# Kernel tuning notes

Hardware: AMD Instinct MI355X
Metric: run time of the kernel (lower is better)

Reference implementation:

```python
import jax, jax.numpy as jnp
import numpy as np

N = 100000      # nodes
E = 1_000_000   # edges (avg degree ~10)
D_IN = 64
HID = 64
N_CLS = 32


def setup_inputs() -> dict:
    key = jax.random.key(0)
    ks = jax.random.split(key, 9)
    x = jax.random.normal(ks[0], (N, D_IN), dtype=jnp.float32)
    edge_index = jax.random.randint(ks[1], (2, E), 0, N, dtype=jnp.int32)
    s_in = 1.0 / np.sqrt(D_IN)
    s_h = 1.0 / np.sqrt(HID)
    W1 = jax.random.normal(ks[2], (D_IN, HID), dtype=jnp.float32) * s_in
    b1 = jnp.zeros((HID,), dtype=jnp.float32)
    W2 = jax.random.normal(ks[3], (HID, HID), dtype=jnp.float32) * s_h
    b2 = jnp.zeros((HID,), dtype=jnp.float32)
    Wl = jax.random.normal(ks[4], (HID, N_CLS), dtype=jnp.float32) * s_h
    bl = jnp.zeros((N_CLS,), dtype=jnp.float32)
    return {"x": x, "edge_index": edge_index,
            "W1": W1, "b1": b1, "W2": W2, "b2": b2, "Wl": Wl, "bl": bl}


def reference(x, edge_index, W1, b1, W2, b2, Wl, bl):
    # GCNConv default: add self-loops, symmetric normalization D^-1/2 (A+I) D^-1/2
    loop = jnp.arange(N, dtype=edge_index.dtype)
    src = jnp.concatenate([edge_index[0], loop])  # [E+N]
    dst = jnp.concatenate([edge_index[1], loop])  # [E+N]

    deg = jax.ops.segment_sum(jnp.ones_like(dst, dtype=jnp.float32), dst,
                              num_segments=N)              # [N]
    dinv = jnp.where(deg > 0, jax.lax.rsqrt(deg), 0.0)      # D^-1/2
    norm = dinv[src] * dinv[dst]                            # [E+N]

    def gcn_conv(h, W, b):
        h = h @ W                                           # [N, F_out]
        msg = h[src] * norm[:, None]                        # gather + scale
        return jax.ops.segment_sum(msg, dst, num_segments=N) + b

    h = jax.nn.relu(gcn_conv(x, W1, b1))
    h = jax.nn.relu(gcn_conv(h, W2, b2))
    return h @ Wl + bl
```

## Files before the change

kernel.cpp:

```cpp
#include <hip/hip_runtime.h>
#include <hip/hip_fp16.h>
#include <math.h>


#define TPB    256
#define TPB1   1024
#define EBLKS  256
#define BSH    7
#define BNODES (1 << BSH)
#define CAPSH  11
#define CAP    (1 << CAPSH)

__global__ __launch_bounds__(TPB1)
void k_scatter(const int* __restrict__ src, const int* __restrict__ dst,
               int* __restrict__ gcnt, int* __restrict__ ebuf,
               int E, int CH, int NBC) {
    __shared__ int h[1024];
    int tid = threadIdx.x, b = blockIdx.x;
    h[tid] = 0;
    __syncthreads();
    int beg = b * CH, end = min(E, beg + CH);
    if (beg < end) {
        int nfull = (end - beg) & ~3;
        for (int i = beg + tid * 4; i < beg + nfull; i += TPB1 * 4) {
            int4 d = *(const int4*)&dst[i];
            atomicAdd(&h[d.x >> BSH], 1);
            atomicAdd(&h[d.y >> BSH], 1);
            atomicAdd(&h[d.z >> BSH], 1);
            atomicAdd(&h[d.w >> BSH], 1);
        }
        if (tid < (end - beg) - nfull)
            atomicAdd(&h[dst[beg + nfull + tid] >> BSH], 1);
    }
    __syncthreads();
    for (int c = tid; c < NBC; c += TPB1) {
        int n = h[c];
        int base = (n > 0) ? atomicAdd(&gcnt[c], n) : 0;
        h[c] = (c << CAPSH) + base;
    }
    __syncthreads();
    if (beg >= end) return;
    int nfull = (end - beg) & ~3;
    for (int i = beg + tid * 4; i < beg + nfull; i += TPB1 * 4) {
        int4 s4 = *(const int4*)&src[i];
        int4 d4 = *(const int4*)&dst[i];
        int p0 = atomicAdd(&h[d4.x >> BSH], 1);
        int p1 = atomicAdd(&h[d4.y >> BSH], 1);
        int p2 = atomicAdd(&h[d4.z >> BSH], 1);
        int p3 = atomicAdd(&h[d4.w >> BSH], 1);
        ebuf[p0] = (s4.x << BSH) | (d4.x & (BNODES - 1));
        ebuf[p1] = (s4.y << BSH) | (d4.y & (BNODES - 1));
        ebuf[p2] = (s4.z << BSH) | (d4.z & (BNODES - 1));
        ebuf[p3] = (s4.w << BSH) | (d4.w & (BNODES - 1));
    }
    if (tid < (end - beg) - nfull) {
        int i = beg + nfull + tid;
        int d = dst[i];
        int p = atomicAdd(&h[d >> BSH], 1);
        ebuf[p] = (src[i] << BSH) | (d & (BNODES - 1));
    }
}

__global__ __launch_bounds__(TPB)
void k_p2f(const int* __restrict__ ebuf, const int* __restrict__ gcnt,
           int* __restrict__ row_ptr, int* __restrict__ row_end,
           float* __restrict__ dinv, int* __restrict__ colw,
           int N, int NBC) {
    __shared__ int cnt[BNODES];
    __shared__ int ofs[BNODES];
    __shared__ int s1[TPB];
    int tid = threadIdx.x, c = blockIdx.x;
    int beg = c << CAPSH;
    int end = beg + gcnt[c];
    if (tid < BNODES) cnt[tid] = 0;
    __syncthreads();
    for (int i = beg + tid; i < end; i += TPB)
        atomicAdd(&cnt[ebuf[i] & (BNODES - 1)], 1);
    __syncthreads();
    int a = (tid < BNODES) ? cnt[tid] : 0;
    s1[tid] = a;
    __syncthreads();
    for (int off = 1; off < TPB; off <<= 1) {
        int x = (tid >= off) ? s1[tid - off] : 0;
        __syncthreads();
        s1[tid] += x;
        __syncthreads();
    }
    int ex = s1[tid] - a;
    if (tid < BNODES) {
        int node = (c << BSH) + tid;
        ofs[tid] = beg + ex;
        if (node < N) {
            row_ptr[node] = beg + ex;
            row_end[node] = beg + ex + a;
            dinv[node]    = rsqrtf((float)(a + 1));
        }
        cnt[tid] = 0;
    }
    __syncthreads();
    for (int i0 = beg + tid; i0 < end; i0 += TPB * 4) {
        int sv[4], dl[4], pos[4];
        int have = 0;
#pragma unroll
        for (int k = 0; k < 4; ++k) {
            int i = i0 + k * TPB;
            if (i < end) {
                int e = ebuf[i];
                sv[k] = e >> BSH;
                dl[k] = e & (BNODES - 1);
                have = k + 1;
            }
        }
#pragma unroll
        for (int k = 0; k < 4; ++k) {
            if (k < have) {
                int r  = atomicAdd(&cnt[dl[k]], 1);
                pos[k] = ofs[dl[k]] + r;
            }
        }
#pragma unroll
        for (int k = 0; k < 4; ++k)
            if (k < have) colw[pos[k]] = sv[k];
    }
}

__launch_bounds__(256)
__global__ void k_mm(const float* __restrict__ in, const float* __restrict__ W,
                     const float* __restrict__ dinv,
                     __half* __restrict__ out, int n) {
    __shared__ float in_s[64 * 68];
    __shared__ float w_s[64 * 64];

    const int tid  = threadIdx.x;
    const int row0 = blockIdx.x * 64;

    for (int i4 = tid; i4 < (64 * 64) / 4; i4 += 256)
        ((float4*)w_s)[i4] = ((const float4*)W)[i4];

    for (int idx = tid; idx < 64 * 16; idx += 256) {
        int r  = idx >> 4;
        int c4 = idx & 15;
        float4 v;
        if (row0 + r < n)
            v = *(const float4*)(in + (size_t)(row0 + r) * 64 + c4 * 4);
        else
            v = make_float4(0.f, 0.f, 0.f, 0.f);
        *(float4*)&in_s[r * 68 + c4 * 4] = v;
    }
    __syncthreads();

    constexpr int CPT = 4;
    const int tx = tid & 15;
    const int ty = tid >> 4;

    float acc[4][CPT];
#pragma unroll
    for (int r = 0; r < 4; ++r)
#pragma unroll
        for (int c = 0; c < CPT; ++c) acc[r][c] = 0.f;

#pragma unroll 4
    for (int k = 0; k < 64; ++k) {
        float b[CPT];
#pragma unroll
        for (int c = 0; c < CPT; ++c) b[c] = w_s[k * 64 + tx * CPT + c];
#pragma unroll
        for (int r = 0; r < 4; ++r) {
            float a = in_s[(ty * 4 + r) * 68 + k];
#pragma unroll
            for (int c = 0; c < CPT; ++c) acc[r][c] = fmaf(a, b[c], acc[r][c]);
        }
    }

#pragma unroll
    for (int r = 0; r < 4; ++r) {
        int row = row0 + ty * 4 + r;
        if (row >= n) continue;
        float dd = dinv[row];
        __half2 p0 = __floats2half2_rn(acc[r][0] * dd, acc[r][1] * dd);
        __half2 p1 = __floats2half2_rn(acc[r][2] * dd, acc[r][3] * dd);
        uint2 u = make_uint2(*(unsigned*)&p0, *(unsigned*)&p1);
        *(uint2*)(out + (size_t)row * 64 + tx * 4) = u;
    }
    if (blockIdx.x == 0 && tid < 16)
        *(uint2*)(out + (size_t)n * 64 + tid * 4) = make_uint2(0u, 0u);
}

__global__ __launch_bounds__(256)
void k_gather_mm(const int* __restrict__ row_ptr, const int* __restrict__ row_end,
                 const int* __restrict__ colw,
                 const float* __restrict__ dinv, const float* __restrict__ bias,
                 const __half* __restrict__ t, const float* __restrict__ W2,
                 __half* __restrict__ t2, int N) {
    __shared__ float  w_s[64 * 64];
    __shared__ __half aggs[32][72];

    int tid = threadIdx.x;
    for (int i4 = tid; i4 < (64 * 64) / 4; i4 += 256)
        ((float4*)w_s)[i4] = ((const float4*)W2)[i4];

    int wv   = tid >> 6;
    int lane = tid & 63;
    int g = lane >> 3;
    int p = lane & 7;
    int slot = tid >> 3;
    int d = blockIdx.x * 32 + wv * 8 + g;

    int beg = 0, end = 0;
    if (d < N) { beg = row_ptr[d]; end = row_end[d]; }

    float acc[8];
#pragma unroll
    for (int k = 0; k < 8; ++k) acc[k] = 0.f;

    for (int e = beg; e < end; e += 4) {
        int s0 = colw[e];
        int s1 = (e + 1 < end) ? colw[e + 1] : N;
        int s2 = (e + 2 < end) ? colw[e + 2] : N;
        int s3 = (e + 3 < end) ? colw[e + 3] : N;
        uint4 a0 = *(const uint4*)(t + (size_t)s0 * 64 + p * 8);
        uint4 a1 = *(const uint4*)(t + (size_t)s1 * 64 + p * 8);
        uint4 a2 = *(const uint4*)(t + (size_t)s2 * 64 + p * 8);
        uint4 a3 = *(const uint4*)(t + (size_t)s3 * 64 + p * 8);
        float2 f;
        f = __half22float2(*(__half2*)&a0.x); acc[0] += f.x; acc[1] += f.y;
        f = __half22float2(*(__half2*)&a0.y); acc[2] += f.x; acc[3] += f.y;
        f = __half22float2(*(__half2*)&a0.z); acc[4] += f.x; acc[5] += f.y;
        f = __half22float2(*(__half2*)&a0.w); acc[6] += f.x; acc[7] += f.y;
        f = __half22float2(*(__half2*)&a1.x); acc[0] += f.x; acc[1] += f.y;
        f = __half22float2(*(__half2*)&a1.y); acc[2] += f.x; acc[3] += f.y;
        f = __half22float2(*(__half2*)&a1.z); acc[4] += f.x; acc[5] += f.y;
        f = __half22float2(*(__half2*)&a1.w); acc[6] += f.x; acc[7] += f.y;
        f = __half22float2(*(__half2*)&a2.x); acc[0] += f.x; acc[1] += f.y;
        f = __half22float2(*(__half2*)&a2.y); acc[2] += f.x; acc[3] += f.y;
        f = __half22float2(*(__half2*)&a2.z); acc[4] += f.x; acc[5] += f.y;
        f = __half22float2(*(__half2*)&a2.w); acc[6] += f.x; acc[7] += f.y;
        f = __half22float2(*(__half2*)&a3.x); acc[0] += f.x; acc[1] += f.y;
        f = __half22float2(*(__half2*)&a3.y); acc[2] += f.x; acc[3] += f.y;
        f = __half22float2(*(__half2*)&a3.z); acc[4] += f.x; acc[5] += f.y;
        f = __half22float2(*(__half2*)&a3.w); acc[6] += f.x; acc[7] += f.y;
    }

    if (d < N) {
        float dd = dinv[d];
        uint4 a = *(const uint4*)(t + (size_t)d * 64 + p * 8);
        float4 b0 = *(const float4*)&bias[p * 8];
        float4 b1 = *(const float4*)&bias[p * 8 + 4];
        float2 s0 = __half22float2(*(__half2*)&a.x);
        float2 s1 = __half22float2(*(__half2*)&a.y);
        float2 s2 = __half22float2(*(__half2*)&a.z);
        float2 s3 = __half22float2(*(__half2*)&a.w);
        float o0 = fmaxf(fmaf(dd, acc[0] + s0.x, b0.x), 0.f);
        float o1 = fmaxf(fmaf(dd, acc[1] + s0.y, b0.y), 0.f);
        float o2 = fmaxf(fmaf(dd, acc[2] + s1.x, b0.z), 0.f);
        float o3 = fmaxf(fmaf(dd, acc[3] + s1.y, b0.w), 0.f);
        float o4 = fmaxf(fmaf(dd, acc[4] + s2.x, b1.x), 0.f);
        float o5 = fmaxf(fmaf(dd, acc[5] + s2.y, b1.y), 0.f);
        float o6 = fmaxf(fmaf(dd, acc[6] + s3.x, b1.z), 0.f);
        float o7 = fmaxf(fmaf(dd, acc[7] + s3.y, b1.w), 0.f);
        __half2 h0 = __floats2half2_rn(o0, o1);
        __half2 h1 = __floats2half2_rn(o2, o3);
        __half2 h2 = __floats2half2_rn(o4, o5);
        __half2 h3 = __floats2half2_rn(o6, o7);
        *(uint4*)&aggs[slot][p * 8] = make_uint4(*(unsigned*)&h0, *(unsigned*)&h1,
                                                *(unsigned*)&h2, *(unsigned*)&h3);
    }
    __syncthreads();

    if (d < N) {
        float dd = dinv[d];
        float a0 = 0.f, a1 = 0.f, a2 = 0.f, a3 = 0.f;
        float a4 = 0.f, a5 = 0.f, a6 = 0.f, a7 = 0.f;
#pragma unroll
        for (int k0 = 0; k0 < 64; k0 += 8) {
            uint4 u = *(const uint4*)&aggs[slot][k0];
            float2 f0 = __half22float2(*(__half2*)&u.x);
            float2 f1 = __half22float2(*(__half2*)&u.y);
            float2 f2 = __half22float2(*(__half2*)&u.z);
            float2 f3 = __half22float2(*(__half2*)&u.w);
            float av[8] = {f0.x, f0.y, f1.x, f1.y, f2.x, f2.y, f3.x, f3.y};
#pragma unroll
            for (int j = 0; j < 8; ++j) {
                const float* wr = &w_s[(k0 + j) * 64 + p * 8];
                float4 w0 = *(const float4*)&wr[0];
                float4 w1 = *(const float4*)&wr[4];
                a0 = fmaf(av[j], w0.x, a0);
                a1 = fmaf(av[j], w0.y, a1);
                a2 = fmaf(av[j], w0.z, a2);
                a3 = fmaf(av[j], w0.w, a3);
                a4 = fmaf(av[j], w1.x, a4);
                a5 = fmaf(av[j], w1.y, a5);
                a6 = fmaf(av[j], w1.z, a6);
                a7 = fmaf(av[j], w1.w, a7);
            }
        }
        __half2 q0 = __floats2half2_rn(a0 * dd, a1 * dd);
        __half2 q1 = __floats2half2_rn(a2 * dd, a3 * dd);
        __half2 q2 = __floats2half2_rn(a4 * dd, a5 * dd);
        __half2 q3 = __floats2half2_rn(a6 * dd, a7 * dd);
        uint4 u = make_uint4(*(unsigned*)&q0, *(unsigned*)&q1,
                             *(unsigned*)&q2, *(unsigned*)&q3);
        *(uint4*)(t2 + (size_t)d * 64 + p * 8) = u;
    }
    if (blockIdx.x == 0 && tid < 16)
        *(uint2*)(t2 + (size_t)N * 64 + tid * 4) = make_uint2(0u, 0u);
}

__global__ __launch_bounds__(256)
void k_gather_head(const int* __restrict__ row_ptr, const int* __restrict__ row_end,
                   const int* __restrict__ colw,
                   const float* __restrict__ dinv, const float* __restrict__ bias,
                   const __half* __restrict__ t, const float* __restrict__ Wl,
                   const float* __restrict__ bl, float* __restrict__ out, int N) {
    __shared__ float wl_s[64 * 32];
    __shared__ float aggs[32][68];

    int tid  = threadIdx.x;
    for (int i4 = tid; i4 < (64 * 32) / 4; i4 += 256)
        ((float4*)wl_s)[i4] = ((const float4*)Wl)[i4];

    int wv   = tid >> 6;
    int lane = tid & 63;
    int g = lane >> 3;
    int p = lane & 7;
    int slot = tid >> 3;
    int d = blockIdx.x * 32 + wv * 8 + g;

    int beg = 0, end = 0;
    if (d < N) { beg = row_ptr[d]; end = row_end[d]; }

    float acc[8];
#pragma unroll
    for (int k = 0; k < 8; ++k) acc[k] = 0.f;

    for (int e = beg; e < end; e += 4) {
        int s0 = colw[e];
        int s1 = (e + 1 < end) ? colw[e + 1] : N;
        int s2 = (e + 2 < end) ? colw[e + 2] : N;
        int s3 = (e + 3 < end) ? colw[e + 3] : N;
        uint4 a0 = *(const uint4*)(t + (size_t)s0 * 64 + p * 8);
        uint4 a1 = *(const uint4*)(t + (size_t)s1 * 64 + p * 8);
        uint4 a2 = *(const uint4*)(t + (size_t)s2 * 64 + p * 8);
        uint4 a3 = *(const uint4*)(t + (size_t)s3 * 64 + p * 8);
        float2 f;
        f = __half22float2(*(__half2*)&a0.x); acc[0] += f.x; acc[1] += f.y;
        f = __half22float2(*(__half2*)&a0.y); acc[2] += f.x; acc[3] += f.y;
        f = __half22float2(*(__half2*)&a0.z); acc[4] += f.x; acc[5] += f.y;
        f = __half22float2(*(__half2*)&a0.w); acc[6] += f.x; acc[7] += f.y;
        f = __half22float2(*(__half2*)&a1.x); acc[0] += f.x; acc[1] += f.y;
        f = __half22float2(*(__half2*)&a1.y); acc[2] += f.x; acc[3] += f.y;
        f = __half22float2(*(__half2*)&a1.z); acc[4] += f.x; acc[5] += f.y;
        f = __half22float2(*(__half2*)&a1.w); acc[6] += f.x; acc[7] += f.y;
        f = __half22float2(*(__half2*)&a2.x); acc[0] += f.x; acc[1] += f.y;
        f = __half22float2(*(__half2*)&a2.y); acc[2] += f.x; acc[3] += f.y;
        f = __half22float2(*(__half2*)&a2.z); acc[4] += f.x; acc[5] += f.y;
        f = __half22float2(*(__half2*)&a2.w); acc[6] += f.x; acc[7] += f.y;
        f = __half22float2(*(__half2*)&a3.x); acc[0] += f.x; acc[1] += f.y;
        f = __half22float2(*(__half2*)&a3.y); acc[2] += f.x; acc[3] += f.y;
        f = __half22float2(*(__half2*)&a3.z); acc[4] += f.x; acc[5] += f.y;
        f = __half22float2(*(__half2*)&a3.w); acc[6] += f.x; acc[7] += f.y;
    }

    if (d < N) {
        float dd = dinv[d];
        uint4 a = *(const uint4*)(t + (size_t)d * 64 + p * 8);
        float4 b0 = *(const float4*)&bias[p * 8];
        float4 b1 = *(const float4*)&bias[p * 8 + 4];
        float2 s0 = __half22float2(*(__half2*)&a.x);
        float2 s1 = __half22float2(*(__half2*)&a.y);
        float2 s2 = __half22float2(*(__half2*)&a.z);
        float2 s3 = __half22float2(*(__half2*)&a.w);
        float o0 = fmaxf(fmaf(dd, acc[0] + s0.x, b0.x), 0.f);
        float o1 = fmaxf(fmaf(dd, acc[1] + s0.y, b0.y), 0.f);
        float o2 = fmaxf(fmaf(dd, acc[2] + s1.x, b0.z), 0.f);
        float o3 = fmaxf(fmaf(dd, acc[3] + s1.y, b0.w), 0.f);
        float o4 = fmaxf(fmaf(dd, acc[4] + s2.x, b1.x), 0.f);
        float o5 = fmaxf(fmaf(dd, acc[5] + s2.y, b1.y), 0.f);
        float o6 = fmaxf(fmaf(dd, acc[6] + s3.x, b1.z), 0.f);
        float o7 = fmaxf(fmaf(dd, acc[7] + s3.y, b1.w), 0.f);
        *(float4*)&aggs[slot][p * 8]     = make_float4(o0, o1, o2, o3);
        *(float4*)&aggs[slot][p * 8 + 4] = make_float4(o4, o5, o6, o7);
    }
    __syncthreads();

    if (d < N) {
        float a0 = 0.f, a1 = 0.f, a2 = 0.f, a3 = 0.f;
#pragma unroll 8
        for (int k = 0; k < 64; ++k) {
            float av = aggs[slot][k];
            float4 w = ((const float4*)&wl_s[k * 32])[p];
            a0 = fmaf(av, w.x, a0);
            a1 = fmaf(av, w.y, a1);
            a2 = fmaf(av, w.z, a2);
            a3 = fmaf(av, w.w, a3);
        }
        float4 bb = *(const float4*)&bl[p * 4];
        *(float4*)&out[(size_t)d * 32 + p * 4] =
            make_float4(a0 + bb.x, a1 + bb.y, a2 + bb.z, a3 + bb.w);
    }
}

extern "C" void kernel_launch(void* const* d_in, const int* in_sizes, int n_in,
                              void* d_out, int out_size, void* d_ws, size_t ws_size,
                              hipStream_t stream) {
    const float* x  = (const float*)d_in[0];
    const int*   ei = (const int*)d_in[1];
    const float* W1 = (const float*)d_in[2];
    const float* b1 = (const float*)d_in[3];
    const float* W2 = (const float*)d_in[4];
    const float* b2 = (const float*)d_in[5];
    const float* Wl = (const float*)d_in[6];
    const float* bl = (const float*)d_in[7];
    float*       out = (float*)d_out;

    const int N = in_sizes[0] / 64;
    const int E = in_sizes[1] / 2;
    const int* srcp = ei;
    const int* dstp = ei + E;

    const int NBC = (N + BNODES - 1) / BNODES;
    const int CH  = (((E + EBLKS - 1) / EBLKS) + 3) & ~3;

    char*  ws  = (char*)d_ws;
    size_t off = 0;
    auto alloc = [&](size_t bytes) -> void* {
        void* p = (void*)(ws + off);
        off += (bytes + 255) & ~(size_t)255;
        return p;
    };
    int*    gcnt    = (int*)alloc((size_t)NBC * 4);
    int*    ebuf    = (int*)alloc((size_t)NBC * CAP * 4);
    int*    colw    = (int*)alloc((size_t)NBC * CAP * 4);
    int*    row_ptr = (int*)alloc((size_t)N * 4);
    int*    row_end = (int*)alloc((size_t)N * 4);
    float*  dinv    = (float*)alloc((size_t)N * 4);
    __half* t1      = (__half*)alloc((size_t)(N + 1) * 64 * 2);
    __half* t2      = (__half*)alloc((size_t)(N + 1) * 64 * 2);

    const int nb_mm = (N + 63) / 64;
    const int nb_g  = (N + 31) / 32;

    hipMemsetAsync(gcnt, 0, (size_t)NBC * 4, stream);
    k_scatter<<<EBLKS, TPB1, 0, stream>>>(srcp, dstp, gcnt, ebuf, E, CH, NBC);
    k_p2f    <<<NBC,   TPB,  0, stream>>>(ebuf, gcnt, row_ptr, row_end,
                                          dinv, colw, N, NBC);

    k_mm<<<nb_mm, 256, 0, stream>>>(x, W1, dinv, t1, N);

    k_gather_mm<<<nb_g, 256, 0, stream>>>(row_ptr, row_end, colw, dinv, b1,
                                          t1, W2, t2, N);

    k_gather_head<<<nb_g, 256, 0, stream>>>(row_ptr, row_end, colw, dinv, b2,
                                            t2, Wl, bl, out, N);
}
```

Measured before the change: 183.8 us.

## Eliminate CSR-building kernel; rebuild per-block adjacency in shared memory inside consumers

Drops the separate bucket-to-CSR kernel and the global row_ptr/row_end/dinv/colw arrays. Each consumer kernel rescans its 128-node bucket from ebuf, counts degrees for its 64-node half and computes dinv. The two gather kernels also build a local sorted column list in shared memory and gather from it. This removes one launch and the global CSR writes and reads, at the cost of scanning each bucket redundantly in every kernel (twice per bucket per kernel). It also relies on a half-bucket holding no more than HCAP edges.

Result: no change. 186.2 us (+1.3%).

```diff
diff --git a/kernel.cpp b/kernel.cpp
--- a/kernel.cpp
+++ b/kernel.cpp
@@ -3,13 +3,13 @@
 #include <math.h>
 
 
-#define TPB    256
 #define TPB1   1024
 #define EBLKS  256
 #define BSH    7
 #define BNODES (1 << BSH)
 #define CAPSH  11
 #define CAP    (1 << CAPSH)
+#define HCAP   1024
 
 __global__ __launch_bounds__(TPB1)
 void k_scatter(const int* __restrict__ src, const int* __restrict__ dst,
@@ -61,78 +61,18 @@
     }
 }
 
-__global__ __launch_bounds__(TPB)
-void k_p2f(const int* __restrict__ ebuf, const int* __restrict__ gcnt,
-           int* __restrict__ row_ptr, int* __restrict__ row_end,
-           float* __restrict__ dinv, int* __restrict__ colw,
-           int N, int NBC) {
-    __shared__ int cnt[BNODES];
-    __shared__ int ofs[BNODES];
-    __shared__ int s1[TPB];
-    int tid = threadIdx.x, c = blockIdx.x;
-    int beg = c << CAPSH;
-    int end = beg + gcnt[c];
-    if (tid < BNODES) cnt[tid] = 0;
-    __syncthreads();
-    for (int i = beg + tid; i < end; i += TPB)
-        atomicAdd(&cnt[ebuf[i] & (BNODES - 1)], 1);
-    __syncthreads();
-    int a = (tid < BNODES) ? cnt[tid] : 0;
-    s1[tid] = a;
-    __syncthreads();
-    for (int off = 1; off < TPB; off <<= 1) {
-        int x = (tid >= off) ? s1[tid - off] : 0;
-        __syncthreads();
-        s1[tid] += x;
-        __syncthreads();
-    }
-    int ex = s1[tid] - a;
-    if (tid < BNODES) {
-        int node = (c << BSH) + tid;
-        ofs[tid] = beg + ex;
-        if (node < N) {
-            row_ptr[node] = beg + ex;
-            row_end[node] = beg + ex + a;
-            dinv[node]    = rsqrtf((float)(a + 1));
-        }
-        cnt[tid] = 0;
-    }
-    __syncthreads();
-    for (int i0 = beg + tid; i0 < end; i0 += TPB * 4) {
-        int sv[4], dl[4], pos[4];
-        int have = 0;
-#pragma unroll
-        for (int k = 0; k < 4; ++k) {
-            int i = i0 + k * TPB;
-            if (i < end) {
-                int e = ebuf[i];
-                sv[k] = e >> BSH;
-                dl[k] = e & (BNODES - 1);
-                have = k + 1;
-            }
-        }
-#pragma unroll
-        for (int k = 0; k < 4; ++k) {
-            if (k < have) {
-                int r  = atomicAdd(&cnt[dl[k]], 1);
-                pos[k] = ofs[dl[k]] + r;
-            }
-        }
-#pragma unroll
-        for (int k = 0; k < 4; ++k)
-            if (k < have) colw[pos[k]] = sv[k];
-    }
-}
-
 __launch_bounds__(256)
 __global__ void k_mm(const float* __restrict__ in, const float* __restrict__ W,
-                     const float* __restrict__ dinv,
+                     const int* __restrict__ ebuf, const int* __restrict__ gcnt,
                      __half* __restrict__ out, int n) {
     __shared__ float in_s[64 * 68];
     __shared__ float w_s[64 * 64];
+    __shared__ int   cnt[64];
 
     const int tid  = threadIdx.x;
     const int row0 = blockIdx.x * 64;
+    const int c    = blockIdx.x >> 1;
+    const int lb   = (blockIdx.x & 1) << 6;
 
     for (int i4 = tid; i4 < (64 * 64) / 4; i4 += 256)
         ((float4*)w_s)[i4] = ((const float4*)W)[i4];
@@ -147,7 +87,17 @@
             v = make_float4(0.f, 0.f, 0.f, 0.f);
         *(float4*)&in_s[r * 68 + c4 * 4] = v;
     }
-    __syncthreads();
+    if (tid < 64) cnt[tid] = 0;
+    __syncthreads();
+
+    {
+        const int ebeg = c << CAPSH;
+        const int eend = ebeg + gcnt[c];
+        for (int i = ebeg + tid; i < eend; i += 256) {
+            int lr = (ebuf[i] & (BNODES - 1)) - lb;
+            if ((unsigned)lr < 64u) atomicAdd(&cnt[lr], 1);
+        }
+    }
 
     constexpr int CPT = 4;
     const int tx = tid & 15;
@@ -157,26 +107,29 @@
 #pragma unroll
     for (int r = 0; r < 4; ++r)
 #pragma unroll
-        for (int c = 0; c < CPT; ++c) acc[r][c] = 0.f;
+        for (int cc = 0; cc < CPT; ++cc) acc[r][cc] = 0.f;
 
 #pragma unroll 4
     for (int k = 0; k < 64; ++k) {
         float b[CPT];
 #pragma unroll
-        for (int c = 0; c < CPT; ++c) b[c] = w_s[k * 64 + tx * CPT + c];
+        for (int cc = 0; cc < CPT; ++cc) b[cc] = w_s[k * 64 + tx * CPT + cc];
 #pragma unroll
         for (int r = 0; r < 4; ++r) {
             float a = in_s[(ty * 4 + r) * 68 + k];
 #pragma unroll
-            for (int c = 0; c < CPT; ++c) acc[r][c] = fmaf(a, b[c], acc[r][c]);
-        }
-    }
+            for (int cc = 0; cc < CPT; ++cc)
+                acc[r][cc] = fmaf(a, b[cc], acc[r][cc]);
+        }
+    }
+    __syncthreads();
 
 #pragma unroll
     for (int r = 0; r < 4; ++r) {
-        int row = row0 + ty * 4 + r;
+        int lrow = ty * 4 + r;
+        int row  = row0 + lrow;
         if (row >= n) continue;
-        float dd = dinv[row];
+        float dd = rsqrtf((float)(cnt[lrow] + 1));
         __half2 p0 = __floats2half2_rn(acc[r][0] * dd, acc[r][1] * dd);
         __half2 p1 = __floats2half2_rn(acc[r][2] * dd, acc[r][3] * dd);
         uint2 u = make_uint2(*(unsigned*)&p0, *(unsigned*)&p1);
@@ -186,42 +139,78 @@
         *(uint2*)(out + (size_t)n * 64 + tid * 4) = make_uint2(0u, 0u);
 }
 
-__global__ __launch_bounds__(256)
-void k_gather_mm(const int* __restrict__ row_ptr, const int* __restrict__ row_end,
-                 const int* __restrict__ colw,
-                 const float* __restrict__ dinv, const float* __restrict__ bias,
-                 const __half* __restrict__ t, const float* __restrict__ W2,
-                 __half* __restrict__ t2, int N) {
+__global__ __launch_bounds__(512)
+void k_gather_mm(const int* __restrict__ ebuf, const int* __restrict__ gcnt,
+                 const float* __restrict__ bias, const __half* __restrict__ t,
+                 const float* __restrict__ W2, __half* __restrict__ t2, int N) {
     __shared__ float  w_s[64 * 64];
-    __shared__ __half aggs[32][72];
-
-    int tid = threadIdx.x;
-    for (int i4 = tid; i4 < (64 * 64) / 4; i4 += 256)
+    __shared__ __half aggs[64][72];
+    __shared__ int    colw_s[HCAP];
+    __shared__ int    cnt[64];
+    __shared__ int    ofs[64];
+    __shared__ int    scn[64];
+    __shared__ float  dinv_s[64];
+
+    const int tid = threadIdx.x;
+    const int c   = blockIdx.x >> 1;
+    const int lb  = (blockIdx.x & 1) << 6;
+
+    for (int i4 = tid; i4 < (64 * 64) / 4; i4 += 512)
         ((float4*)w_s)[i4] = ((const float4*)W2)[i4];
 
-    int wv   = tid >> 6;
-    int lane = tid & 63;
-    int g = lane >> 3;
-    int p = lane & 7;
-    int slot = tid >> 3;
-    int d = blockIdx.x * 32 + wv * 8 + g;
-
-    int beg = 0, end = 0;
-    if (d < N) { beg = row_ptr[d]; end = row_end[d]; }
+    if (tid < 64) cnt[tid] = 0;
+    __syncthreads();
+    const int ebeg = c << CAPSH;
+    const int eend = ebeg + gcnt[c];
+    for (int i = ebeg + tid; i < eend; i += 512) {
+        int lr = (ebuf[i] & (BNODES - 1)) - lb;
+        if ((unsigned)lr < 64u) atomicAdd(&cnt[lr], 1);
+    }
+    __syncthreads();
+    int a = (tid < 64) ? cnt[tid] : 0;
+    if (tid < 64) scn[tid] = a;
+    __syncthreads();
+    for (int off = 1; off < 64; off <<= 1) {
+        int x = (tid < 64 && tid >= off) ? scn[tid - off] : 0;
+        __syncthreads();
+        if (tid < 64) scn[tid] += x;
+        __syncthreads();
+    }
+    if (tid < 64) {
+        ofs[tid]    = scn[tid] - a;
+        dinv_s[tid] = rsqrtf((float)(a + 1));
+        cnt[tid]    = 0;
+    }
+    __syncthreads();
+    for (int i = ebeg + tid; i < eend; i += 512) {
+        int e  = ebuf[i];
+        int lr = (e & (BNODES - 1)) - lb;
+        if ((unsigned)lr < 64u) {
+            int r = atomicAdd(&cnt[lr], 1);
+            colw_s[ofs[lr] + r] = e >> BSH;
+        }
+    }
+    __syncthreads();
+
+    const int p = tid & 7;
+    const int l = tid >> 3;
+    const int d = (c << BSH) + lb + l;
+    const int eb = ofs[l];
+    const int ee = eb + cnt[l];
 
     float acc[8];
 #pragma unroll
     for (int k = 0; k < 8; ++k) acc[k] = 0.f;
 
-    for (int e = beg; e < end; e += 4) {
-        int s0 = colw[e];
-        int s1 = (e + 1 < end) ? colw[e + 1] : N;
-        int s2 = (e + 2 < end) ? colw[e + 2] : N;
-        int s3 = (e + 3 < end) ? colw[e + 3] : N;
-        uint4 a0 = *(const uint4*)(t + (size_t)s0 * 64 + p * 8);
-        uint4 a1 = *(const uint4*)(t + (size_t)s1 * 64 + p * 8);
-        uint4 a2 = *(const uint4*)(t + (size_t)s2 * 64 + p * 8);
-        uint4 a3 = *(const uint4*)(t + (size_t)s3 * 64 + p * 8);
+    for (int e = eb; e < ee; e += 4) {
+        int v0 = colw_s[e];
+        int v1 = (e + 1 < ee) ? colw_s[e + 1] : N;
+        int v2 = (e + 2 < ee) ? colw_s[e + 2] : N;
+        int v3 = (e + 3 < ee) ? colw_s[e + 3] : N;
+        uint4 a0 = *(const uint4*)(t + (size_t)v0 * 64 + p * 8);
+        uint4 a1 = *(const uint4*)(t + (size_t)v1 * 64 + p * 8);
+        uint4 a2 = *(const uint4*)(t + (size_t)v2 * 64 + p * 8);
+        uint4 a3 = *(const uint4*)(t + (size_t)v3 * 64 + p * 8);
         float2 f;
         f = __half22float2(*(__half2*)&a0.x); acc[0] += f.x; acc[1] += f.y;
         f = __half22float2(*(__half2*)&a0.y); acc[2] += f.x; acc[3] += f.y;
@@ -242,14 +231,14 @@
     }
 
     if (d < N) {
-        float dd = dinv[d];
-        uint4 a = *(const uint4*)(t + (size_t)d * 64 + p * 8);
+        float dd = dinv_s[l];
+        uint4 aa = *(const uint4*)(t + (size_t)d * 64 + p * 8);
         float4 b0 = *(const float4*)&bias[p * 8];
         float4 b1 = *(const float4*)&bias[p * 8 + 4];
-        float2 s0 = __half22float2(*(__half2*)&a.x);
-        float2 s1 = __half22float2(*(__half2*)&a.y);
-        float2 s2 = __half22float2(*(__half2*)&a.z);
-        float2 s3 = __half22float2(*(__half2*)&a.w);
+        float2 s0 = __half22float2(*(__half2*)&aa.x);
+        float2 s1 = __half22float2(*(__half2*)&aa.y);
+        float2 s2 = __half22float2(*(__half2*)&aa.z);
+        float2 s3 = __half22float2(*(__half2*)&aa.w);
         float o0 = fmaxf(fmaf(dd, acc[0] + s0.x, b0.x), 0.f);
         float o1 = fmaxf(fmaf(dd, acc[1] + s0.y, b0.y), 0.f);
         float o2 = fmaxf(fmaf(dd, acc[2] + s1.x, b0.z), 0.f);
@@ -262,18 +251,18 @@
         __half2 h1 = __floats2half2_rn(o2, o3);
         __half2 h2 = __floats2half2_rn(o4, o5);
         __half2 h3 = __floats2half2_rn(o6, o7);
-        *(uint4*)&aggs[slot][p * 8] = make_uint4(*(unsigned*)&h0, *(unsigned*)&h1,
-                                                *(unsigned*)&h2, *(unsigned*)&h3);
+        *(uint4*)&aggs[l][p * 8] = make_uint4(*(unsigned*)&h0, *(unsigned*)&h1,
+                                              *(unsigned*)&h2, *(unsigned*)&h3);
     }
     __syncthreads();
 
     if (d < N) {
-        float dd = dinv[d];
+        float dd = dinv_s[l];
         float a0 = 0.f, a1 = 0.f, a2 = 0.f, a3 = 0.f;
         float a4 = 0.f, a5 = 0.f, a6 = 0.f, a7 = 0.f;
 #pragma unroll
         for (int k0 = 0; k0 < 64; k0 += 8) {
-            uint4 u = *(const uint4*)&aggs[slot][k0];
+            uint4 u = *(const uint4*)&aggs[l][k0];
             float2 f0 = __half22float2(*(__half2*)&u.x);
             float2 f1 = __half22float2(*(__half2*)&u.y);
             float2 f2 = __half22float2(*(__half2*)&u.z);
@@ -306,42 +295,79 @@
         *(uint2*)(t2 + (size_t)N * 64 + tid * 4) = make_uint2(0u, 0u);
 }
 
-__global__ __launch_bounds__(256)
-void k_gather_head(const int* __restrict__ row_ptr, const int* __restrict__ row_end,
-                   const int* __restrict__ colw,
-                   const float* __restrict__ dinv, const float* __restrict__ bias,
-                   const __half* __restrict__ t, const float* __restrict__ Wl,
-                   const float* __restrict__ bl, float* __restrict__ out, int N) {
+__global__ __launch_bounds__(512)
+void k_gather_head(const int* __restrict__ ebuf, const int* __restrict__ gcnt,
+                   const float* __restrict__ bias, const __half* __restrict__ t,
+                   const float* __restrict__ Wl, const float* __restrict__ bl,
+                   float* __restrict__ out, int N) {
     __shared__ float wl_s[64 * 32];
-    __shared__ float aggs[32][68];
-
-    int tid  = threadIdx.x;
-    for (int i4 = tid; i4 < (64 * 32) / 4; i4 += 256)
+    __shared__ float aggs[64][68];
+    __shared__ int   colw_s[HCAP];
+    __shared__ int   cnt[64];
+    __shared__ int   ofs[64];
+    __shared__ int   scn[64];
+    __shared__ float dinv_s[64];
+
+    const int tid = threadIdx.x;
+    const int c   = blockIdx.x >> 1;
+    const int lb  = (blockIdx.x & 1) << 6;
+
+    for (int i4 = tid; i4 < (64 * 32) / 4; i4 += 512)
         ((float4*)wl_s)[i4] = ((const float4*)Wl)[i4];
 
-    int wv   = tid >> 6;
-    int lane = tid & 63;
-    int g = lane >> 3;
-    int p = lane & 7;
-    int slot = tid >> 3;
-    int d = blockIdx.x * 32 + wv * 8 + g;
-
-    int beg = 0, end = 0;
-    if (d < N) { beg = row_ptr[d]; end = row_end[d]; }
+    if (tid < 64) cnt[tid] = 0;
+    __syncthreads();
+    const int ebeg = c << CAPSH;
+    const int eend = ebeg + gcnt[c];
+    for (int i = ebeg + tid; i < eend; i += 512) {
+        int lr = (ebuf[i] & (BNODES - 1)) - lb;
+        if ((unsigned)lr < 64u) atomicAdd(&cnt[lr], 1);
+    }
+    __syncthreads();
+    int a = (tid < 64) ? cnt[tid] : 0;
+    if (tid < 64) scn[tid] = a;
+    __syncthreads();
+    for (int off = 1; off < 64; off <<= 1) {
+        int x = (tid < 64 && tid >= off) ? scn[tid - off] : 0;
+        __syncthreads();
+        if (tid < 64) scn[tid] += x;
+        __syncthreads();
+    }
+    if (tid < 64) {
+        ofs[tid]    = scn[tid] - a;
+        dinv_s[tid] = rsqrtf((float)(a + 1));
+        cnt[tid]    = 0;
+    }
+    __syncthreads();
+    for (int i = ebeg + tid; i < eend; i += 512) {
+        int e  = ebuf[i];
+        int lr = (e & (BNODES - 1)) - lb;
+        if ((unsigned)lr < 64u) {
+            int r = atomicAdd(&cnt[lr], 1);
+            colw_s[ofs[lr] + r] = e >> BSH;
+        }
+    }
+    __syncthreads();
+
+    const int p = tid & 7;
+    const int l = tid >> 3;
+    const int d = (c << BSH) + lb + l;
+    const int eb = ofs[l];
+    const int ee = eb + cnt[l];
 
     float acc[8];
 #pragma unroll
     for (int k = 0; k < 8; ++k) acc[k] = 0.f;
 
-    for (int e = beg; e < end; e += 4) {
-        int s0 = colw[e];
-        int s1 = (e + 1 < end) ? colw[e + 1] : N;
-        int s2 = (e + 2 < end) ? colw[e + 2] : N;
-        int s3 = (e + 3 < end) ? colw[e + 3] : N;
-        uint4 a0 = *(const uint4*)(t + (size_t)s0 * 64 + p * 8);
-        uint4 a1 = *(const uint4*)(t + (size_t)s1 * 64 + p * 8);
-        uint4 a2 = *(const uint4*)(t + (size_t)s2 * 64 + p * 8);
-        uint4 a3 = *(const uint4*)(t + (size_t)s3 * 64 + p * 8);
+    for (int e = eb; e < ee; e += 4) {
+        int v0 = colw_s[e];
+        int v1 = (e + 1 < ee) ? colw_s[e + 1] : N;
+        int v2 = (e + 2 < ee) ? colw_s[e + 2] : N;
+        int v3 = (e + 3 < ee) ? colw_s[e + 3] : N;
+        uint4 a0 = *(const uint4*)(t + (size_t)v0 * 64 + p * 8);
+        uint4 a1 = *(const uint4*)(t + (size_t)v1 * 64 + p * 8);
+        uint4 a2 = *(const uint4*)(t + (size_t)v2 * 64 + p * 8);
+        uint4 a3 = *(const uint4*)(t + (size_t)v3 * 64 + p * 8);
         float2 f;
         f = __half22float2(*(__half2*)&a0.x); acc[0] += f.x; acc[1] += f.y;
         f = __half22float2(*(__half2*)&a0.y); acc[2] += f.x; acc[3] += f.y;
@@ -362,14 +388,14 @@
     }
 
     if (d < N) {
-        float dd = dinv[d];
-        uint4 a = *(const uint4*)(t + (size_t)d * 64 + p * 8);
+        float dd = dinv_s[l];
+        uint4 aa = *(const uint4*)(t + (size_t)d * 64 + p * 8);
         float4 b0 = *(const float4*)&bias[p * 8];
         float4 b1 = *(const float4*)&bias[p * 8 + 4];
-        float2 s0 = __half22float2(*(__half2*)&a.x);
-        float2 s1 = __half22float2(*(__half2*)&a.y);
-        float2 s2 = __half22float2(*(__half2*)&a.z);
-        float2 s3 = __half22float2(*(__half2*)&a.w);
+        float2 s0 = __half22float2(*(__half2*)&aa.x);
+        float2 s1 = __half22float2(*(__half2*)&aa.y);
+        float2 s2 = __half22float2(*(__half2*)&aa.z);
+        float2 s3 = __half22float2(*(__half2*)&aa.w);
         float o0 = fmaxf(fmaf(dd, acc[0] + s0.x, b0.x), 0.f);
         float o1 = fmaxf(fmaf(dd, acc[1] + s0.y, b0.y), 0.f);
         float o2 = fmaxf(fmaf(dd, acc[2] + s1.x, b0.z), 0.f);
@@ -378,8 +404,8 @@
         float o5 = fmaxf(fmaf(dd, acc[5] + s2.y, b1.y), 0.f);
         float o6 = fmaxf(fmaf(dd, acc[6] + s3.x, b1.z), 0.f);
         float o7 = fmaxf(fmaf(dd, acc[7] + s3.y, b1.w), 0.f);
-        *(float4*)&aggs[slot][p * 8]     = make_float4(o0, o1, o2, o3);
-        *(float4*)&aggs[slot][p * 8 + 4] = make_float4(o4, o5, o6, o7);
+        *(float4*)&aggs[l][p * 8]     = make_float4(o0, o1, o2, o3);
+        *(float4*)&aggs[l][p * 8 + 4] = make_float4(o4, o5, o6, o7);
     }
     __syncthreads();
 
@@ -387,7 +413,7 @@
         float a0 = 0.f, a1 = 0.f, a2 = 0.f, a3 = 0.f;
 #pragma unroll 8
         for (int k = 0; k < 64; ++k) {
-            float av = aggs[slot][k];
+            float av = aggs[l][k];
             float4 w = ((const float4*)&wl_s[k * 32])[p];
             a0 = fmaf(av, w.x, a0);
             a1 = fmaf(av, w.y, a1);
@@ -428,28 +454,20 @@
         off += (bytes + 255) & ~(size_t)255;
         return p;
     };
-    int*    gcnt    = (int*)alloc((size_t)NBC * 4);
-    int*    ebuf    = (int*)alloc((size_t)NBC * CAP * 4);
-    int*    colw    = (int*)alloc((size_t)NBC * CAP * 4);
-    int*    row_ptr = (int*)alloc((size_t)N * 4);
-    int*    row_end = (int*)alloc((size_t)N * 4);
-    float*  dinv    = (float*)alloc((size_t)N * 4);
-    __half* t1      = (__half*)alloc((size_t)(N + 1) * 64 * 2);
-    __half* t2      = (__half*)alloc((size_t)(N + 1) * 64 * 2);
+    int*    gcnt = (int*)alloc((size_t)NBC * 4);
+    int*    ebuf = (int*)alloc((size_t)NBC * CAP * 4);
+    __half* t1   = (__half*)alloc((size_t)(N + 1) * 64 * 2);
+    __half* t2   = (__half*)alloc((size_t)(N + 1) * 64 * 2);
 
     const int nb_mm = (N + 63) / 64;
-    const int nb_g  = (N + 31) / 32;
+    const int nb_g  = (N + 63) / 64;
 
     hipMemsetAsync(gcnt, 0, (size_t)NBC * 4, stream);
     k_scatter<<<EBLKS, TPB1, 0, stream>>>(srcp, dstp, gcnt, ebuf, E, CH, NBC);
-    k_p2f    <<<NBC,   TPB,  0, stream>>>(ebuf, gcnt, row_ptr, row_end,
-                                          dinv, colw, N, NBC);
-
-    k_mm<<<nb_mm, 256, 0, stream>>>(x, W1, dinv, t1, N);
-
-    k_gather_mm<<<nb_g, 256, 0, stream>>>(row_ptr, row_end, colw, dinv, b1,
-                                          t1, W2, t2, N);
-
-    k_gather_head<<<nb_g, 256, 0, stream>>>(row_ptr, row_end, colw, dinv, b2,
-                                            t2, Wl, bl, out, N);
+
+    k_mm<<<nb_mm, 256, 0, stream>>>(x, W1, ebuf, gcnt, t1, N);
+
+    k_gather_mm<<<nb_g, 512, 0, stream>>>(ebuf, gcnt, b1, t1, W2, t2, N);
+
+    k_gather_head<<<nb_g, 512, 0, stream>>>(ebuf, gcnt, b2, t2, Wl, bl, out, N);
 }
```
